# Kernel tuning notes

Measured on AMD Instinct MI355X. Metric: run time of the kernel, lower is better.

## Reference

```python
import jax, jax.numpy as jnp
import numpy as np


def setup_inputs() -> dict:
    key = jax.random.key(0)
    ks = jax.random.split(key, 12)
    N_DRUGS, D, N_CELLS, C_IN, E = 4096, 128, 1024, 1000, 500000
    inp = {
        "drug_hidden_out": jax.random.normal(ks[0], (N_DRUGS, D), dtype=jnp.float32),
        "cell_hidden_out": jax.random.normal(ks[1], (N_CELLS, C_IN), dtype=jnp.float32),
        # columns: drug1_idx, drug2_idx, cell_idx, label (original code indexes
        # drug_hidden_out with ALL THREE index columns, so bound by N_DRUGS)
        "all_edges": jax.random.randint(ks[2], (E, 4), 0, N_DRUGS, dtype=jnp.int64),
        # proj: Linear(1000, 128)
        "proj_W": jax.random.normal(ks[3], (D, C_IN), dtype=jnp.float32) * 0.03,
        "proj_b": jnp.zeros((D,), dtype=jnp.float32),
        # NN: Linear(128,32) -> ReLU -> Linear(32,32) -> ReLU -> Linear(32,32)
        #     -> ReLU -> Dropout(eval=identity) -> Linear(32,1) -> Sigmoid
        "W1": jax.random.normal(ks[4], (32, D), dtype=jnp.float32) * 0.08,
        "b1": jnp.zeros((32,), dtype=jnp.float32),
        "W2": jax.random.normal(ks[5], (32, 32), dtype=jnp.float32) * 0.17,
        "b2": jnp.zeros((32,), dtype=jnp.float32),
        "W3": jax.random.normal(ks[6], (32, 32), dtype=jnp.float32) * 0.17,
        "b3": jnp.zeros((32,), dtype=jnp.float32),
        "W4": jax.random.normal(ks[7], (1, 32), dtype=jnp.float32) * 0.17,
        "b4": jnp.zeros((1,), dtype=jnp.float32),
    }
    return inp


def reference(drug_hidden_out, cell_hidden_out, all_edges,
              proj_W, proj_b, W1, b1, W2, b2, W3, b3, W4, b4):
    # proj is computed in the original forward but its result is never used
    # downstream (the code re-indexes drug_hidden_out for cell_fea).
    _cell_proj = cell_hidden_out @ proj_W.T + proj_b  # [n_cells, 128], dead value

    edges = all_edges.T                 # [4, E]
    label = edges[3]                    # [E]
    edge_index = edges[:3]              # [3, E]

    drug1_fea = drug_hidden_out[edge_index[0]]   # [E, 128] gather
    drug2_fea = drug_hidden_out[edge_index[1]]   # [E, 128] gather
    cell_fea = drug_hidden_out[edge_index[2]]    # [E, 128] gather (faithful to source bug)
    logits = drug1_fea * drug2_fea * cell_fea    # [E, 128]

    h = jax.nn.relu(logits @ W1.T + b1)          # [E, 32]
    h = jax.nn.relu(h @ W2.T + b2)               # [E, 32]
    h = jax.nn.relu(h @ W3.T + b3)               # [E, 32] (dropout = identity in eval)
    x = jax.nn.sigmoid(h @ W4.T + b4)            # [E, 1]
    return x, label
```

## Files before the change

### kernel.cpp

```cpp
#include <hip/hip_runtime.h>
#include <stdint.h>

#define DD 128
#define HH 32
#define RS 36
#define TABQ (4096 * DD / 4)
#define BLOB_OFF (1u << 20)

typedef _Float16 f16;
typedef _Float16 f16x4 __attribute__((ext_vector_type(4)));
typedef _Float16 f16x8 __attribute__((ext_vector_type(8)));
typedef float    f32x4 __attribute__((ext_vector_type(4)));

__global__ __launch_bounds__(256)
void synergy_prepass(const float* __restrict__ drug,
                     const float* __restrict__ W1, const float* __restrict__ W2,
                     const float* __restrict__ W3, const float* __restrict__ W4,
                     f16* __restrict__ tab)
{
    const int tid = threadIdx.x;
    if ((int)blockIdx.x == 512) {
        f16x8* __restrict__ blob16 = (f16x8*)((char*)tab + BLOB_OFF);
        const float4* __restrict__ W1v = (const float4*)W1;
        #pragma unroll
        for (int p = 0; p < 2; ++p) {
            const int S = p * 256 + tid;
            const int t = S >> 8, f = (S >> 6) & 3, l = S & 63;
            const int mm = l & 15, qq = l >> 4;
            const int c4 = (t * 16 + mm) * (DD / 4) + f * 8 + qq * 2;
            const float4 w0 = W1v[c4], w1 = W1v[c4 + 1];
            f16x8 r;
            r[0]=(f16)w0.x; r[1]=(f16)w0.y; r[2]=(f16)w0.z; r[3]=(f16)w0.w;
            r[4]=(f16)w1.x; r[5]=(f16)w1.y; r[6]=(f16)w1.z; r[7]=(f16)w1.w;
            blob16[S] = r;
        }
        {
            const int B = tid & 127;
            const int t = B >> 6, l = B & 63;
            const int mm = l & 15, qq = l >> 4;
            const int c4 = (t * 16 + mm) * (HH / 4) + qq * 2;
            const float4* __restrict__ src = (tid < 128) ? (const float4*)W2 : (const float4*)W3;
            const float4 w0 = src[c4], w1 = src[c4 + 1];
            f16x8 r;
            r[0]=(f16)w0.x; r[1]=(f16)w0.y; r[2]=(f16)w0.z; r[3]=(f16)w0.w;
            r[4]=(f16)w1.x; r[5]=(f16)w1.y; r[6]=(f16)w1.z; r[7]=(f16)w1.w;
            blob16[512 + (tid & 128) + B] = r;
        }
        if (tid < 64) {
            const int mm = tid & 15, qq = tid >> 4;
            f16x8 r;
            #pragma unroll
            for (int j = 0; j < 8; ++j)
                r[j] = (mm == 0) ? (f16)W4[qq * 8 + j] : (f16)0.0f;
            blob16[768 + tid] = r;
        }
        return;
    }
    const int i = blockIdx.x * 256 + tid;
    if (i < TABQ) {
        const float4 v = ((const float4*)drug)[i];
        f16x4 h;
        h[0]=(f16)v.x; h[1]=(f16)v.y; h[2]=(f16)v.z; h[3]=(f16)v.w;
        ((f16x4*)tab)[i] = h;
    }
}

__global__ __launch_bounds__(256, 4)
void synergy_main(const f16* __restrict__ tab, const int* __restrict__ edges,
                  const float* __restrict__ b1, const float* __restrict__ b2,
                  const float* __restrict__ b3, const float* __restrict__ b4,
                  float* __restrict__ out, int E, int NG)
{
    __shared__ __align__(16) f16 stage[4][12 * 1088 / 2];

    const int tid  = threadIdx.x;
    const int wave = tid >> 6;
    const int lane = tid & 63;
    const int m    = lane & 15;
    const int q    = lane >> 4;
    const int mq   = lane >> 4;
    const int sg   = lane & 15;

    const int WSTR = (int)gridDim.x * 4;
    int g = (int)blockIdx.x * 4 + wave;
    if (g >= NG) return;

    const char* __restrict__ tabB   = (const char*)tab;
    const int4* __restrict__ edges4 = (const int4*)edges;

    const f16x8* __restrict__ blobG = (const f16x8*)(tabB + BLOB_OFF);
    f16x8 wa[2][4];
    #pragma unroll
    for (int t = 0; t < 2; ++t)
        #pragma unroll
        for (int f = 0; f < 4; ++f)
            wa[t][f] = blobG[(t * 4 + f) * 64 + lane];
    const f16x8 w2a = blobG[512 + lane], w2b = blobG[576 + lane];
    const f16x8 w3a = blobG[640 + lane], w3b = blobG[704 + lane];
    const f16x8 wf4 = blobG[768 + lane];
    const float b1a = b1[m], b1b = b1[16 + m];
    const float b2a = b2[m], b2b = b2[16 + m];
    const float b3a = b3[m], b3b = b3[16 + m];
    const float b4v = b4[0];

    f16* __restrict__ stg = stage[wave];
    f16* __restrict__ hb  = stg;

    auto load_ed = [&](int gg) -> int4 {
        int e = (gg << 4) + m;
        e = (e < E) ? e : (E - 1);
        return edges4[e];
    };
    f16x8 dat[12];
    auto issue_loads = [&](const int4 ed) {
        #pragma unroll
        for (int s = 0; s < 12; ++s) {
            const int src = 4 * (s & 3) + mq;
            const int t = s >> 2;
            const int row = (t == 0) ? __shfl(ed.x, src, 64)
                          : (t == 1) ? __shfl(ed.y, src, 64)
                                     : __shfl(ed.z, src, 64);
            dat[s] = *(const f16x8*)(tabB + ((size_t)row << 8) + (sg << 4));
        }
    };

    int4 ed_cur = load_ed(g);
    issue_loads(ed_cur);
    int gn = g + WSTR;
    int4 ed_nxt = load_ed((gn < NG) ? gn : g);

    const int woff  = mq * 272 + sg * 16;
    const int rbase = (m >> 2) * 1088 + (m & 3) * 272 + (q << 4);

    for (;;) {
        #pragma unroll
        for (int s = 0; s < 12; ++s)
            *(f16x8*)((char*)stg + s * 1088 + woff) = dat[s];

        issue_loads(ed_nxt);
        const int gf = gn + WSTR;
        const int4 ed_fut = load_ed((gf < NG) ? gf : g);

        f32x4 acc0 = {b1a, b1a, b1a, b1a};
        f32x4 acc1 = {b1b, b1b, b1b, b1b};
        #pragma unroll
        for (int f = 0; f < 4; ++f) {
            const int off = rbase + f * 64;
            const f16x8 v0 = *(const f16x8*)((char*)stg + off);
            const f16x8 v1 = *(const f16x8*)((char*)stg + off + 4352);
            const f16x8 v2 = *(const f16x8*)((char*)stg + off + 8704);
            const f16x8 p = v0 * v1 * v2;
            acc0 = __builtin_amdgcn_mfma_f32_16x16x32_f16(p, wa[0][f], acc0, 0, 0, 0);
            acc1 = __builtin_amdgcn_mfma_f32_16x16x32_f16(p, wa[1][f], acc1, 0, 0, 0);
        }
        #pragma unroll
        for (int r = 0; r < 4; ++r) {
            const int row = 4 * q + r;
            hb[row * RS + m]      = (f16)fmaxf(acc0[r], 0.0f);
            hb[row * RS + 16 + m] = (f16)fmaxf(acc1[r], 0.0f);
        }

        {
            const f16x8 a2 = *(const f16x8*)(hb + m * RS + q * 8);
            f32x4 c0 = {b2a, b2a, b2a, b2a};
            f32x4 c1 = {b2b, b2b, b2b, b2b};
            c0 = __builtin_amdgcn_mfma_f32_16x16x32_f16(a2, w2a, c0, 0, 0, 0);
            c1 = __builtin_amdgcn_mfma_f32_16x16x32_f16(a2, w2b, c1, 0, 0, 0);
            #pragma unroll
            for (int r = 0; r < 4; ++r) {
                const int row = 4 * q + r;
                hb[row * RS + m]      = (f16)fmaxf(c0[r], 0.0f);
                hb[row * RS + 16 + m] = (f16)fmaxf(c1[r], 0.0f);
            }
        }

        {
            const f16x8 a3 = *(const f16x8*)(hb + m * RS + q * 8);
            f32x4 d0 = {b3a, b3a, b3a, b3a};
            f32x4 d1 = {b3b, b3b, b3b, b3b};
            d0 = __builtin_amdgcn_mfma_f32_16x16x32_f16(a3, w3a, d0, 0, 0, 0);
            d1 = __builtin_amdgcn_mfma_f32_16x16x32_f16(a3, w3b, d1, 0, 0, 0);
            #pragma unroll
            for (int r = 0; r < 4; ++r) {
                const int row = 4 * q + r;
                hb[row * RS + m]      = (f16)fmaxf(d0[r], 0.0f);
                hb[row * RS + 16 + m] = (f16)fmaxf(d1[r], 0.0f);
            }
        }

        {
            const f16x8 a4 = *(const f16x8*)(hb + m * RS + q * 8);
            f32x4 z = {b4v, b4v, b4v, b4v};
            z = __builtin_amdgcn_mfma_f32_16x16x32_f16(a4, wf4, z, 0, 0, 0);
            if (m == 0) {
                const int e0 = (g << 4) + 4 * q;
                float4 res;
                res.x = 1.0f / (1.0f + __expf(-z[0]));
                res.y = 1.0f / (1.0f + __expf(-z[1]));
                res.z = 1.0f / (1.0f + __expf(-z[2]));
                res.w = 1.0f / (1.0f + __expf(-z[3]));
                if (e0 + 3 < E) *(float4*)(out + e0) = res;
                else {
                    if (e0 + 0 < E) out[e0 + 0] = res.x;
                    if (e0 + 1 < E) out[e0 + 1] = res.y;
                    if (e0 + 2 < E) out[e0 + 2] = res.z;
                }
            }
        }
        const int eL = (g << 4) + lane;
        if (lane < 16 && eL < E) out[E + eL] = (float)ed_cur.w;

        if (gn >= NG) break;
        g = gn; gn = gf; ed_cur = ed_nxt; ed_nxt = ed_fut;
    }
}

extern "C" void kernel_launch(void* const* d_in, const int* in_sizes, int n_in,
                              void* d_out, int out_size, void* d_ws, size_t ws_size,
                              hipStream_t stream)
{
    const float* drug  = (const float*)d_in[0];
    const int*   edges = (const int*)d_in[2];
    const float* W1 = (const float*)d_in[5];
    const float* b1 = (const float*)d_in[6];
    const float* W2 = (const float*)d_in[7];
    const float* b2 = (const float*)d_in[8];
    const float* W3 = (const float*)d_in[9];
    const float* b3 = (const float*)d_in[10];
    const float* W4 = (const float*)d_in[11];
    const float* b4 = (const float*)d_in[12];
    float* out = (float*)d_out;
    f16*   tab = (f16*)d_ws;

    const int E  = in_sizes[2] / 4;
    const int NG = (E + 15) / 16;

    hipLaunchKernelGGL(synergy_prepass, dim3(513), dim3(256), 0, stream,
                       drug, W1, W2, W3, W4, tab);
    int blocks = (NG + 3) / 4;
    if (blocks > 768) blocks = 768;
    hipLaunchKernelGGL(synergy_main, dim3(blocks), dim3(256), 0, stream,
                       tab, edges, b1, b2, b3, b4, out, E, NG);
}
```

Before: 122.9 us.

## Gather edge rows directly into MFMA operand layout, drop LDS staging

Each lane now loads its own edge's drug rows in the layout the first MFMA expects, so the 12-slot LDS staging buffer and the per-load shuffles go away. The hidden-layer buffer is repacked as f16 pairs with a matching K permutation applied to W2, W3 and W4 in the prepass. The next group's gathers are issued after the first-layer MFMAs, and the grid cap is raised from 768 to 1024 blocks. Each lane now reads a 16-byte segment from a different random row, which may make the gathers less coalesced than the old row-contiguous pattern.

```diff
diff --git a/kernel.cpp b/kernel.cpp
--- a/kernel.cpp
+++ b/kernel.cpp
@@ -3,14 +3,16 @@
 
 #define DD 128
 #define HH 32
-#define RS 36
+#define RS32 20
 #define TABQ (4096 * DD / 4)
 #define BLOB_OFF (1u << 20)
 
 typedef _Float16 f16;
+typedef _Float16 f16x2 __attribute__((ext_vector_type(2)));
 typedef _Float16 f16x4 __attribute__((ext_vector_type(4)));
 typedef _Float16 f16x8 __attribute__((ext_vector_type(8)));
 typedef float    f32x4 __attribute__((ext_vector_type(4)));
+
 
 __global__ __launch_bounds__(256)
 void synergy_prepass(const float* __restrict__ drug,
@@ -38,20 +40,24 @@
             const int B = tid & 127;
             const int t = B >> 6, l = B & 63;
             const int mm = l & 15, qq = l >> 4;
-            const int c4 = (t * 16 + mm) * (HH / 4) + qq * 2;
-            const float4* __restrict__ src = (tid < 128) ? (const float4*)W2 : (const float4*)W3;
-            const float4 w0 = src[c4], w1 = src[c4 + 1];
+            const float* __restrict__ src = (tid < 128) ? W2 : W3;
+            const int n = t * 16 + mm;
             f16x8 r;
-            r[0]=(f16)w0.x; r[1]=(f16)w0.y; r[2]=(f16)w0.z; r[3]=(f16)w0.w;
-            r[4]=(f16)w1.x; r[5]=(f16)w1.y; r[6]=(f16)w1.z; r[7]=(f16)w1.w;
+            #pragma unroll
+            for (int j = 0; j < 8; ++j) {
+                const int kk = ((j & 1) ? 16 : 0) + 4 * qq + (j >> 1);
+                r[j] = (f16)src[n * HH + kk];
+            }
             blob16[512 + (tid & 128) + B] = r;
         }
         if (tid < 64) {
             const int mm = tid & 15, qq = tid >> 4;
             f16x8 r;
             #pragma unroll
-            for (int j = 0; j < 8; ++j)
-                r[j] = (mm == 0) ? (f16)W4[qq * 8 + j] : (f16)0.0f;
+            for (int j = 0; j < 8; ++j) {
+                const int kk = ((j & 1) ? 16 : 0) + 4 * qq + (j >> 1);
+                r[j] = (mm == 0) ? (f16)W4[kk] : (f16)0.0f;
+            }
             blob16[768 + tid] = r;
         }
         return;
@@ -71,15 +77,13 @@
                   const float* __restrict__ b3, const float* __restrict__ b4,
                   float* __restrict__ out, int E, int NG)
 {
-    __shared__ __align__(16) f16 stage[4][12 * 1088 / 2];
+    __shared__ __align__(16) f16x2 hbuf[4][16 * RS32];
 
     const int tid  = threadIdx.x;
     const int wave = tid >> 6;
     const int lane = tid & 63;
     const int m    = lane & 15;
     const int q    = lane >> 4;
-    const int mq   = lane >> 4;
-    const int sg   = lane & 15;
 
     const int WSTR = (int)gridDim.x * 4;
     int g = (int)blockIdx.x * 4 + wave;
@@ -103,8 +107,7 @@
     const float b3a = b3[m], b3b = b3[16 + m];
     const float b4v = b4[0];
 
-    f16* __restrict__ stg = stage[wave];
-    f16* __restrict__ hb  = stg;
+    f16x2* __restrict__ hb = hbuf[wave];
 
     auto load_ed = [&](int gg) -> int4 {
         int e = (gg << 4) + m;
@@ -113,83 +116,79 @@
     };
     f16x8 dat[12];
     auto issue_loads = [&](const int4 ed) {
-        #pragma unroll
-        for (int s = 0; s < 12; ++s) {
-            const int src = 4 * (s & 3) + mq;
-            const int t = s >> 2;
-            const int row = (t == 0) ? __shfl(ed.x, src, 64)
-                          : (t == 1) ? __shfl(ed.y, src, 64)
-                                     : __shfl(ed.z, src, 64);
-            dat[s] = *(const f16x8*)(tabB + ((size_t)row << 8) + (sg << 4));
+        const int qo = q << 4;
+        const size_t rx = (size_t)ed.x << 8;
+        const size_t ry = (size_t)ed.y << 8;
+        const size_t rz = (size_t)ed.z << 8;
+        #pragma unroll
+        for (int f = 0; f < 4; ++f) {
+            dat[f * 3 + 0] = *(const f16x8*)(tabB + rx + f * 64 + qo);
+            dat[f * 3 + 1] = *(const f16x8*)(tabB + ry + f * 64 + qo);
+            dat[f * 3 + 2] = *(const f16x8*)(tabB + rz + f * 64 + qo);
         }
     };
 
-    int4 ed_cur = load_ed(g);
-    issue_loads(ed_cur);
+    int4 ed0 = load_ed(g);
+    issue_loads(ed0);
+    float lbl = (float)ed0.w;
     int gn = g + WSTR;
-    int4 ed_nxt = load_ed((gn < NG) ? gn : g);
-
-    const int woff  = mq * 272 + sg * 16;
-    const int rbase = (m >> 2) * 1088 + (m & 3) * 272 + (q << 4);
+    int4 ed1 = load_ed((gn < NG) ? gn : g);
 
     for (;;) {
-        #pragma unroll
-        for (int s = 0; s < 12; ++s)
-            *(f16x8*)((char*)stg + s * 1088 + woff) = dat[s];
-
-        issue_loads(ed_nxt);
-        const int gf = gn + WSTR;
-        const int4 ed_fut = load_ed((gf < NG) ? gf : g);
-
         f32x4 acc0 = {b1a, b1a, b1a, b1a};
         f32x4 acc1 = {b1b, b1b, b1b, b1b};
         #pragma unroll
         for (int f = 0; f < 4; ++f) {
-            const int off = rbase + f * 64;
-            const f16x8 v0 = *(const f16x8*)((char*)stg + off);
-            const f16x8 v1 = *(const f16x8*)((char*)stg + off + 4352);
-            const f16x8 v2 = *(const f16x8*)((char*)stg + off + 8704);
-            const f16x8 p = v0 * v1 * v2;
+            const f16x8 p = dat[f * 3 + 0] * dat[f * 3 + 1] * dat[f * 3 + 2];
             acc0 = __builtin_amdgcn_mfma_f32_16x16x32_f16(p, wa[0][f], acc0, 0, 0, 0);
             acc1 = __builtin_amdgcn_mfma_f32_16x16x32_f16(p, wa[1][f], acc1, 0, 0, 0);
         }
+
+        const float lblN = (float)ed1.w;
+        if (gn < NG) issue_loads(ed1);
+        const int gf = gn + WSTR;
+        const int4 ed2 = load_ed((gf < NG) ? gf : g);
+
         #pragma unroll
         for (int r = 0; r < 4; ++r) {
-            const int row = 4 * q + r;
-            hb[row * RS + m]      = (f16)fmaxf(acc0[r], 0.0f);
-            hb[row * RS + 16 + m] = (f16)fmaxf(acc1[r], 0.0f);
-        }
-
-        {
-            const f16x8 a2 = *(const f16x8*)(hb + m * RS + q * 8);
+            f16x2 v;
+            v[0] = (f16)fmaxf(acc0[r], 0.0f);
+            v[1] = (f16)fmaxf(acc1[r], 0.0f);
+            hb[(4 * q + r) * RS32 + m] = v;
+        }
+
+        {
+            const f16x8 a2 = *(const f16x8*)&hb[m * RS32 + q * 4];
             f32x4 c0 = {b2a, b2a, b2a, b2a};
             f32x4 c1 = {b2b, b2b, b2b, b2b};
             c0 = __builtin_amdgcn_mfma_f32_16x16x32_f16(a2, w2a, c0, 0, 0, 0);
             c1 = __builtin_amdgcn_mfma_f32_16x16x32_f16(a2, w2b, c1, 0, 0, 0);
             #pragma unroll
             for (int r = 0; r < 4; ++r) {
-                const int row = 4 * q + r;
-                hb[row * RS + m]      = (f16)fmaxf(c0[r], 0.0f);
-                hb[row * RS + 16 + m] = (f16)fmaxf(c1[r], 0.0f);
-            }
-        }
-
-        {
-            const f16x8 a3 = *(const f16x8*)(hb + m * RS + q * 8);
+                f16x2 v;
+                v[0] = (f16)fmaxf(c0[r], 0.0f);
+                v[1] = (f16)fmaxf(c1[r], 0.0f);
+                hb[(4 * q + r) * RS32 + m] = v;
+            }
+        }
+
+        {
+            const f16x8 a3 = *(const f16x8*)&hb[m * RS32 + q * 4];
             f32x4 d0 = {b3a, b3a, b3a, b3a};
             f32x4 d1 = {b3b, b3b, b3b, b3b};
             d0 = __builtin_amdgcn_mfma_f32_16x16x32_f16(a3, w3a, d0, 0, 0, 0);
             d1 = __builtin_amdgcn_mfma_f32_16x16x32_f16(a3, w3b, d1, 0, 0, 0);
             #pragma unroll
             for (int r = 0; r < 4; ++r) {
-                const int row = 4 * q + r;
-                hb[row * RS + m]      = (f16)fmaxf(d0[r], 0.0f);
-                hb[row * RS + 16 + m] = (f16)fmaxf(d1[r], 0.0f);
-            }
-        }
-
-        {
-            const f16x8 a4 = *(const f16x8*)(hb + m * RS + q * 8);
+                f16x2 v;
+                v[0] = (f16)fmaxf(d0[r], 0.0f);
+                v[1] = (f16)fmaxf(d1[r], 0.0f);
+                hb[(4 * q + r) * RS32 + m] = v;
+            }
+        }
+
+        {
+            const f16x8 a4 = *(const f16x8*)&hb[m * RS32 + q * 4];
             f32x4 z = {b4v, b4v, b4v, b4v};
             z = __builtin_amdgcn_mfma_f32_16x16x32_f16(a4, wf4, z, 0, 0, 0);
             if (m == 0) {
@@ -208,10 +207,10 @@
             }
         }
         const int eL = (g << 4) + lane;
-        if (lane < 16 && eL < E) out[E + eL] = (float)ed_cur.w;
+        if (lane < 16 && eL < E) out[E + eL] = lbl;
 
         if (gn >= NG) break;
-        g = gn; gn = gf; ed_cur = ed_nxt; ed_nxt = ed_fut;
+        g = gn; gn = gf; lbl = lblN; ed1 = ed2;
     }
 }
 
@@ -238,7 +237,7 @@
     hipLaunchKernelGGL(synergy_prepass, dim3(513), dim3(256), 0, stream,
                        drug, W1, W2, W3, W4, tab);
     int blocks = (NG + 3) / 4;
-    if (blocks > 768) blocks = 768;
+    if (blocks > 1024) blocks = 1024;
     hipLaunchKernelGGL(synergy_main, dim3(blocks), dim3(256), 0, stream,
                        tab, edges, b1, b2, b3, b4, out, E, NG);
 }
```

Result: slower. 160.3 us (+30.4%).
